# Kernel tuning notes

Hardware: AMD Instinct MI355X
Metric: run time of the kernel (lower is better)

## Reference

```python
import jax, jax.numpy as jnp
import numpy as np

N = 50000   # nodes
E = 800000  # edges
G = 64      # graphs in batch
D = 128     # joint_embed_dim
H = D // 2  # 64
NEG_SLOPE = 0.2


def _segment_softmax(logits, seg, n):
    m = jax.ops.segment_max(logits, seg, num_segments=n)
    m = jnp.where(jnp.isfinite(m), m, 0.0)
    e = jnp.exp(logits - m[seg])
    s = jax.ops.segment_sum(e, seg, num_segments=n)
    return e / (s[seg] + 1e-16)


def _gat_conv(x, src, dst, W, a_src, a_dst, b, n):
    # PyG GATConv, heads=1, add_self_loops=True
    loops = jnp.arange(n, dtype=src.dtype)
    s = jnp.concatenate([src, loops])
    d = jnp.concatenate([dst, loops])
    h = x @ W                                   # [n, out]
    alpha_s = h @ a_src                         # [n]
    alpha_d = h @ a_dst
    logit = jax.nn.leaky_relu(alpha_s[s] + alpha_d[d], NEG_SLOPE)  # [E+n]
    alpha = _segment_softmax(logit, d, n)
    out = jax.ops.segment_sum(h[s] * alpha[:, None], d, num_segments=n)
    return out + b


def _edge_conv(x, src, dst, We1, be1, We2, be2, n):
    # PyG EdgeConv: max_j nn(cat[x_i, x_j - x_i])
    xi = x[dst]
    xj = x[src]
    feats = jnp.concatenate([xi, xj - xi], axis=1)     # [E, 2*H]
    m = jax.nn.relu(feats @ We1 + be1)
    m = jax.nn.relu(m @ We2 + be2)
    out = jax.ops.segment_max(m, dst, num_segments=n)
    return jnp.where(jnp.isfinite(out), out, 0.0)


def setup_inputs() -> dict:
    key = jax.random.key(0)
    ks = jax.random.split(key, 24)
    x = jax.random.normal(ks[0], (N, 3), dtype=jnp.float32)
    edge_index = jax.random.randint(ks[1], (2, E), 0, N, dtype=jnp.int64)
    batch_ids = jnp.sort(jax.random.randint(ks[2], (N,), 0, G, dtype=jnp.int64))

    def w(k, shape, fan_in):
        return jax.random.normal(k, shape, dtype=jnp.float32) * (1.0 / np.sqrt(fan_in))

    inp = {
        "x": x, "edge_index": edge_index, "batch_ids": batch_ids,
        # GATConv1: 3 -> 64
        "W1": w(ks[3], (3, H), 3), "a1s": w(ks[4], (H,), H), "a1d": w(ks[5], (H,), H), "b1": jnp.zeros((H,), jnp.float32),
        # GATConv2: 64 -> 64
        "W2": w(ks[6], (H, H), H), "a2s": w(ks[7], (H,), H), "a2d": w(ks[8], (H,), H), "b2": jnp.zeros((H,), jnp.float32),
        # GATConv3: 128 -> 128
        "W3": w(ks[9], (D, D), D), "a3s": w(ks[10], (D,), D), "a3d": w(ks[11], (D,), D), "b3": jnp.zeros((D,), jnp.float32),
        # EdgeConv nn: 128 -> 128 -> 128
        "We1": w(ks[12], (D, D), D), "be1": jnp.zeros((D,), jnp.float32),
        "We2": w(ks[13], (D, D), D), "be2": jnp.zeros((D,), jnp.float32),
        # MLP: 256 -> 128 -> 128
        "Wm1": w(ks[14], (2 * D, D), 2 * D), "bm1": jnp.zeros((D,), jnp.float32),
        "Wm2": w(ks[15], (D, D), D), "bm2": jnp.zeros((D,), jnp.float32),
    }
    return inp


def reference(x, edge_index, batch_ids,
              W1, a1s, a1d, b1, W2, a2s, a2d, b2, W3, a3s, a3d, b3,
              We1, be1, We2, be2, Wm1, bm1, Wm2, bm2):
    src, dst = edge_index[0], edge_index[1]
    n = x.shape[0]
    # conv1 + relu (dropout is identity in eval)
    h = jax.nn.relu(_gat_conv(x, src, dst, W1, a1s, a1d, b1, n))
    # conv2 + elu
    h = jax.nn.elu(_gat_conv(h, src, dst, W2, a2s, a2d, b2, n))
    # edge_conv: 64 -> 128
    h = _edge_conv(h, src, dst, We1, be1, We2, be2, n)
    # conv3 + relu
    h = jax.nn.relu(_gat_conv(h, src, dst, W3, a3s, a3d, b3, n))
    # global mean / max pool over graphs
    sums = jax.ops.segment_sum(h, batch_ids, num_segments=G)
    cnts = jax.ops.segment_sum(jnp.ones((n, 1), h.dtype), batch_ids, num_segments=G)
    mean_pool = sums / jnp.maximum(cnts, 1.0)
    max_pool = jax.ops.segment_max(h, batch_ids, num_segments=G)
    max_pool = jnp.where(jnp.isfinite(max_pool), max_pool, 0.0)
    z = jnp.concatenate([mean_pool, max_pool], axis=1)    # [G, 256]
    z = jax.nn.relu(z @ Wm1 + bm1)
    z = jax.nn.relu(z @ Wm2 + bm2)
    norm = jnp.linalg.norm(z, axis=1, keepdims=True)
    return z / jnp.maximum(norm, 1e-12)
```

## Files before the change

kernel.cpp:

```cpp
#include <hip/hip_runtime.h>
#include <hip/hip_bf16.h>
#include <math.h>


typedef __attribute__((ext_vector_type(4))) float f32x4;
typedef __attribute__((ext_vector_type(8))) short bf16x8;
typedef __attribute__((ext_vector_type(8))) ushort u16x8;
typedef short s16x2 __attribute__((ext_vector_type(2)));

__device__ __forceinline__ float wave_sum(float v) {
#pragma unroll
  for (int o = 32; o > 0; o >>= 1) v += __shfl_xor(v, o, 64);
  return v;
}
__device__ __forceinline__ float half_sum(float v) {
#pragma unroll
  for (int o = 16; o > 0; o >>= 1) v += __shfl_xor(v, o, 64);
  return v;
}
__device__ __forceinline__ float half_max(float v) {
#pragma unroll
  for (int o = 16; o > 0; o >>= 1) v = fmaxf(v, __shfl_xor(v, o, 64));
  return v;
}
__device__ __forceinline__ float lrelu(float x) { return x >= 0.f ? x : 0.2f * x; }
__device__ __forceinline__ ushort f2bf(float f) {
  union { float f; unsigned u; } v; v.f = f;
  unsigned r = (v.u + 0x7fff + ((v.u >> 16) & 1)) >> 16;
  return (ushort)r;
}
__device__ __forceinline__ float bf2f(ushort u) {
  union { unsigned u; float f; } v; v.u = ((unsigned)u) << 16;
  return v.f;
}
__device__ __forceinline__ float bflo(unsigned v) { return __uint_as_float(v << 16); }
__device__ __forceinline__ float bfhi(unsigned v) { return __uint_as_float(v & 0xffff0000u); }
__device__ __forceinline__ unsigned pack2bf(float a, float b) {
  __hip_bfloat162 h = __float22bfloat162_rn(make_float2(a, b));
  union { __hip_bfloat162 h; unsigned u; } cv;
  cv.h = h;
  return cv.u;
}
__device__ __forceinline__ unsigned bfadd2_relu(unsigned a, unsigned b) {
  union { unsigned u; __hip_bfloat162 h; s16x2 s; } ua, ub, ur;
  ua.u = a;
  ub.u = b;
  ur.h = __hadd2(ua.h, ub.h);
  s16x2 z = (s16x2)0;
  ur.s = __builtin_elementwise_max(ur.s, z);
  return ur.u;
}


__global__ void count_kernel(const int* __restrict__ ei, int* __restrict__ deg, int E) {
  int e = blockIdx.x * 256 + threadIdx.x;
  if (e < E) atomicAdd(&deg[ei[E + e]], 1);
}

__global__ void scan_local(const int* __restrict__ deg, int* __restrict__ off,
                           int* __restrict__ bsum, int n) {
  __shared__ int buf[256];
  int i = blockIdx.x * 256 + threadIdx.x;
  int v = (i < n) ? deg[i] : 0;
  buf[threadIdx.x] = v;
  __syncthreads();
  int incl = v;
  for (int o = 1; o < 256; o <<= 1) {
    int t = (threadIdx.x >= o) ? buf[threadIdx.x - o] : 0;
    __syncthreads();
    incl += t;
    buf[threadIdx.x] = incl;
    __syncthreads();
  }
  if (i < n) off[i] = incl - v;
  if (threadIdx.x == 255) bsum[blockIdx.x] = incl;
}

__global__ void scan_bsum(int* __restrict__ bsum, int nb) {
  __shared__ int buf[256];
  int v = (threadIdx.x < nb) ? bsum[threadIdx.x] : 0;
  buf[threadIdx.x] = v;
  __syncthreads();
  int incl = v;
  for (int o = 1; o < 256; o <<= 1) {
    int t = (threadIdx.x >= o) ? buf[threadIdx.x - o] : 0;
    __syncthreads();
    incl += t;
    buf[threadIdx.x] = incl;
    __syncthreads();
  }
  if (threadIdx.x < nb) bsum[threadIdx.x] = incl - v;
}

__global__ void scan_add(int* __restrict__ off, const int* __restrict__ bsum, int n, int total) {
  int i = blockIdx.x * 256 + threadIdx.x;
  if (i < n) off[i] += bsum[blockIdx.x];
  if (i == 0) off[n] = total;
}

__global__ void scatter_kernel(const int* __restrict__ ei, const int* __restrict__ off,
                               int* __restrict__ cursor, int* __restrict__ csr_src,
                               int* __restrict__ csr_dst, int E) {
  int e = blockIdx.x * 256 + threadIdx.x;
  if (e < E) {
    int d = ei[E + e];
    int pos = off[d] + atomicAdd(&cursor[d], 1);
    csr_src[pos] = ei[e];
    csr_dst[pos] = d;
  }
}


template <int IN, int OUT>
__global__ __launch_bounds__(256) void node_linear_kernel(
    const float* __restrict__ x, const float* __restrict__ W,
    const float* __restrict__ av_s, const float* __restrict__ av_d,
    ushort* __restrict__ hb, float* __restrict__ as_out, float* __restrict__ ad_out, int n) {
  constexpr int NC = OUT / 64;
  constexpr int NB = 4;
  __shared__ float Wl[IN * OUT];
  if constexpr ((IN * OUT) % 1024 == 0) {
    for (int i = threadIdx.x; i < IN * OUT / 4; i += 256)
      ((float4*)Wl)[i] = ((const float4*)W)[i];
  } else {
    for (int i = threadIdx.x; i < IN * OUT; i += 256) Wl[i] = W[i];
  }
  __syncthreads();
  const int wid = threadIdx.x >> 6, lane = threadIdx.x & 63;
  const int n0 = (blockIdx.x * 4 + wid) * NB;
  if (n0 >= n) return;
  float acc[NB][NC];
#pragma unroll
  for (int j = 0; j < NB; ++j)
#pragma unroll
    for (int c = 0; c < NC; ++c) acc[j][c] = 0.f;
  int nidx[NB];
#pragma unroll
  for (int j = 0; j < NB; ++j) nidx[j] = min(n0 + j, n - 1);

  if constexpr ((IN & 3) == 0) {
#pragma unroll 2
    for (int k = 0; k < IN; k += 4) {
      float4 xv[NB];
#pragma unroll
      for (int j = 0; j < NB; ++j) xv[j] = *(const float4*)&x[nidx[j] * IN + k];
#pragma unroll
      for (int kk = 0; kk < 4; ++kk) {
        float w[NC];
        if constexpr (NC == 2) {
          float2 wv = *(const float2*)&Wl[(k + kk) * OUT + 2 * lane];
          w[0] = wv.x;
          w[1] = wv.y;
        } else {
          w[0] = Wl[(k + kk) * OUT + lane];
        }
#pragma unroll
        for (int j = 0; j < NB; ++j) {
          float xk = (kk == 0) ? xv[j].x : (kk == 1) ? xv[j].y : (kk == 2) ? xv[j].z : xv[j].w;
#pragma unroll
          for (int c = 0; c < NC; ++c) acc[j][c] += xk * w[c];
        }
      }
    }
  } else {
    for (int k = 0; k < IN; ++k) {
      float w[NC];
#pragma unroll
      for (int c = 0; c < NC; ++c) w[c] = (NC == 2) ? Wl[k * OUT + 2 * lane + c] : Wl[k * OUT + lane];
#pragma unroll
      for (int j = 0; j < NB; ++j) {
        float xk = x[nidx[j] * IN + k];
#pragma unroll
        for (int c = 0; c < NC; ++c) acc[j][c] += xk * w[c];
      }
    }
  }

  float a_sv[NC], a_dv[NC];
#pragma unroll
  for (int c = 0; c < NC; ++c) {
    const int col = (NC == 2) ? 2 * lane + c : lane;
    a_sv[c] = av_s[col];
    a_dv[c] = av_d[col];
  }
#pragma unroll
  for (int j = 0; j < NB; ++j) {
    int node = n0 + j;
    if (node >= n) break;
    float ps = 0.f, pd = 0.f;
#pragma unroll
    for (int c = 0; c < NC; ++c) {
      ps += acc[j][c] * a_sv[c];
      pd += acc[j][c] * a_dv[c];
    }
    if constexpr (NC == 2) {
      unsigned pk = pack2bf(acc[j][0], acc[j][1]);
      *(unsigned*)&hb[(size_t)node * OUT + 2 * lane] = pk;
    } else {
      hb[(size_t)node * OUT + lane] = f2bf(acc[j][0]);
    }
    ps = wave_sum(ps);
    pd = wave_sum(pd);
    if (lane == 0) {
      as_out[node] = ps;
      ad_out[node] = pd;
    }
  }
}


template <int K>
__global__ void compute_wa(const float* __restrict__ W, const float* __restrict__ a_s,
                           const float* __restrict__ a_d, float* __restrict__ wa_s,
                           float* __restrict__ wa_d) {
  const int k = threadIdx.x;
  float s = 0.f, d = 0.f;
  for (int j = 0; j < K; ++j) {
    const float w = W[k * K + j];
    s += w * a_s[j];
    d += w * a_d[j];
  }
  wa_s[k] = s;
  wa_d[k] = d;
}


#define NT 64
#define M1S 136
#define M2S 132

__global__ __launch_bounds__(256, 4) void node_mfma_kernel(
    const float* __restrict__ x, const ushort* __restrict__ Wcm,
    const float* __restrict__ wa_s, const float* __restrict__ wa_d,
    ushort* __restrict__ hb, float* __restrict__ as_out, float* __restrict__ ad_out, int n) {
  __shared__ __align__(16) char smem[NT * M2S * 4];
  __shared__ float swa[128], swd[128];
  ushort* m1 = (ushort*)smem;
  float* m2 = (float*)smem;
  const int tid = threadIdx.x;
  const int lane = tid & 63, wid = tid >> 6;
  const int quad = lane >> 4, l16 = lane & 15;
  const int row = tid >> 2, c0 = (tid & 3) * 32;

  bf16x8 bfrag[2][4];
#pragma unroll
  for (int ct = 0; ct < 2; ++ct) {
    const int nn = wid * 32 + ct * 16 + l16;
#pragma unroll
    for (int ks = 0; ks < 4; ++ks)
      bfrag[ct][ks] = *(const bf16x8*)&Wcm[nn * 128 + ks * 32 + quad * 8];
  }
  if (tid < 128) {
    swa[tid] = wa_s[tid];
    swd[tid] = wa_d[tid];
  }
  __syncthreads();

  const int n0 = blockIdx.x * NT;
  const int node = min(n0 + row, n - 1);

  float ps = 0.f, pd = 0.f;
  {
    const float4* xp = (const float4*)&x[(size_t)node * 128 + c0];
#pragma unroll
    for (int i = 0; i < 4; ++i) {
      const float4 a = xp[2 * i], b = xp[2 * i + 1];
      const float4 wa0 = *(const float4*)&swa[c0 + 8 * i];
      const float4 wa1 = *(const float4*)&swa[c0 + 8 * i + 4];
      const float4 wd0 = *(const float4*)&swd[c0 + 8 * i];
      const float4 wd1 = *(const float4*)&swd[c0 + 8 * i + 4];
      ps += a.x * wa0.x + a.y * wa0.y + a.z * wa0.z + a.w * wa0.w
          + b.x * wa1.x + b.y * wa1.y + b.z * wa1.z + b.w * wa1.w;
      pd += a.x * wd0.x + a.y * wd0.y + a.z * wd0.z + a.w * wd0.w
          + b.x * wd1.x + b.y * wd1.y + b.z * wd1.z + b.w * wd1.w;
      uint4 rr;
      rr.x = pack2bf(a.x, a.y);
      rr.y = pack2bf(a.z, a.w);
      rr.z = pack2bf(b.x, b.y);
      rr.w = pack2bf(b.z, b.w);
      *((uint4*)&m1[row * M1S + c0] + i) = rr;
    }
  }
  ps += __shfl_xor(ps, 1, 64);
  ps += __shfl_xor(ps, 2, 64);
  pd += __shfl_xor(pd, 1, 64);
  pd += __shfl_xor(pd, 2, 64);
  if ((tid & 3) == 0 && n0 + row < n) {
    as_out[n0 + row] = ps;
    ad_out[n0 + row] = pd;
  }
  __syncthreads();

  f32x4 acc[4][2];
#pragma unroll
  for (int rt = 0; rt < 4; ++rt)
#pragma unroll
    for (int ct = 0; ct < 2; ++ct) acc[rt][ct] = (f32x4)0.f;
#pragma unroll
  for (int ks = 0; ks < 4; ++ks) {
    bf16x8 afr[4];
#pragma unroll
    for (int rt = 0; rt < 4; ++rt)
      afr[rt] = *(const bf16x8*)&m1[(rt * 16 + l16) * M1S + ks * 32 + quad * 8];
#pragma unroll
    for (int rt = 0; rt < 4; ++rt)
#pragma unroll
// ... 47 lines not shown
#pragma unroll
  for (int ks = 0; ks < 2; ++ks)
    bfrag[ks] = *(const bf16x8*)&Wcm[(wid * 16 + l16) * 64 + ks * 32 + quad * 8];
  if (tid < 64) {
    swa[tid] = wa_s[tid];
    swd[tid] = wa_d[tid];
  }
  __syncthreads();

  const int n0 = blockIdx.x * NT;
  const int node = min(n0 + row, n - 1);

  float ps = 0.f, pd = 0.f;
  {
    const float4* xp = (const float4*)&x[(size_t)node * 64 + c0];
#pragma unroll
    for (int i = 0; i < 2; ++i) {
      const float4 a = xp[2 * i], b = xp[2 * i + 1];
      const float4 wa0 = *(const float4*)&swa[c0 + 8 * i];
      const float4 wa1 = *(const float4*)&swa[c0 + 8 * i + 4];
      const float4 wd0 = *(const float4*)&swd[c0 + 8 * i];
      const float4 wd1 = *(const float4*)&swd[c0 + 8 * i + 4];
      ps += a.x * wa0.x + a.y * wa0.y + a.z * wa0.z + a.w * wa0.w
          + b.x * wa1.x + b.y * wa1.y + b.z * wa1.z + b.w * wa1.w;
      pd += a.x * wd0.x + a.y * wd0.y + a.z * wd0.z + a.w * wd0.w
          + b.x * wd1.x + b.y * wd1.y + b.z * wd1.z + b.w * wd1.w;
      uint4 rr;
      rr.x = pack2bf(a.x, a.y);
      rr.y = pack2bf(a.z, a.w);
      rr.z = pack2bf(b.x, b.y);
      rr.w = pack2bf(b.z, b.w);
      *((uint4*)&m1[row * M1S64 + c0] + i) = rr;
    }
  }
  ps += __shfl_xor(ps, 1, 64);
  ps += __shfl_xor(ps, 2, 64);
  pd += __shfl_xor(pd, 1, 64);
  pd += __shfl_xor(pd, 2, 64);
  if ((tid & 3) == 0 && n0 + row < n) {
    as_out[n0 + row] = ps;
    ad_out[n0 + row] = pd;
  }
  __syncthreads();

  f32x4 acc[4];
#pragma unroll
  for (int rt = 0; rt < 4; ++rt) acc[rt] = (f32x4)0.f;
#pragma unroll
  for (int ks = 0; ks < 2; ++ks) {
    bf16x8 afr[4];
#pragma unroll
    for (int rt = 0; rt < 4; ++rt)
      afr[rt] = *(const bf16x8*)&m1[(rt * 16 + l16) * M1S64 + ks * 32 + quad * 8];
#pragma unroll
    for (int rt = 0; rt < 4; ++rt)
      acc[rt] = __builtin_amdgcn_mfma_f32_16x16x32_bf16(afr[rt], bfrag[ks], acc[rt], 0, 0, 0);
  }
  __syncthreads();

  {
    const int col = wid * 16 + l16;
#pragma unroll
    for (int rt = 0; rt < 4; ++rt)
#pragma unroll
      for (int r = 0; r < 4; ++r) {
        const int rr2 = rt * 16 + quad * 4 + r;
        m2[rr2 * M2S64 + col] = acc[rt][r];
      }
  }
  __syncthreads();

  unsigned* hbu = (unsigned*)hb;
#pragma unroll
  for (int i = 0; i < 8; ++i) {
    const int r = wid * 2 + (lane >> 5) + 8 * i;
    const int j = lane & 31;
    if (n0 + r < n)
      hbu[(size_t)(n0 + r) * 32 + j] =
          pack2bf(m2[r * M2S64 + 2 * j], m2[r * M2S64 + 2 * j + 1]);
  }
}


template <int ACT>
__global__ __launch_bounds__(256) void gat_agg128h_kernel(
    const ushort* __restrict__ h, const float* __restrict__ as_, const float* __restrict__ ad_,
    const float* __restrict__ bias, const int* __restrict__ off, const int* __restrict__ csr_src,
    float* __restrict__ out, int n) {
  __shared__ float wbuf[4][64];
  __shared__ int sbuf[4][64];
  const int wid = threadIdx.x >> 6, lane = threadIdx.x & 63;
  const int half = lane >> 5, sl = lane & 31;
  const int d0 = blockIdx.x * 8 + wid * 2 + half;
  const bool wr = d0 < n;
  const int d = wr ? d0 : (n - 1);
  const int s0 = off[d], s1 = off[d + 1];
  const float ad = ad_[d];
  const float l_self = lrelu(as_[d] + ad);
  const uint2 selfv = *(const uint2*)&h[(size_t)d * 128 + 4 * sl];

  float m = l_self;
  float esum_l = 0.f, acc0 = 0.f, acc1 = 0.f, acc2 = 0.f, acc3 = 0.f;

  for (int base = s0; base < s1; base += 32) {
    const int cnt = min(32, s1 - base);
    const int idx = base + sl;
    float l = -3.0e38f;
    int s_l = 0;
    if (idx < s1) {
      s_l = csr_src[idx];
      l = lrelu(as_[s_l] + ad);
    }
    const float cm = half_max(l);
    const float alpha = (cm > m) ? __expf(m - cm) : 1.f;
    esum_l *= alpha;
    acc0 *= alpha;
    acc1 *= alpha;
    acc2 *= alpha;
    acc3 *= alpha;
    m = fmaxf(m, cm);
    const float w_l = (idx < s1) ? __expf(l - m) : 0.f;
    sbuf[wid][half * 32 + sl] = s_l;
    wbuf[wid][half * 32 + sl] = w_l;
    esum_l += w_l;
    __threadfence_block();
    int j = 0;
    for (; j + 8 <= cnt; j += 8) {
      float w[8];
      int a[8];
#pragma unroll
      for (int t = 0; t < 8; ++t) {
        w[t] = wbuf[wid][half * 32 + j + t];
        a[t] = sbuf[wid][half * 32 + j + t];
      }
      uint2 v[8];
#pragma unroll
      for (int t = 0; t < 8; ++t) v[t] = *(const uint2*)&h[(size_t)a[t] * 128 + 4 * sl];
#pragma unroll
      for (int t = 0; t < 8; ++t) {
        acc0 += w[t] * bflo(v[t].x);
        acc1 += w[t] * bfhi(v[t].x);
        acc2 += w[t] * bflo(v[t].y);
        acc3 += w[t] * bfhi(v[t].y);
      }
    }
    for (; j < cnt; ++j) {
      const float wj = wbuf[wid][half * 32 + j];
      const int aj = sbuf[wid][half * 32 + j];
      const uint2 v = *(const uint2*)&h[(size_t)aj * 128 + 4 * sl];
      acc0 += wj * bflo(v.x);
      acc1 += wj * bfhi(v.x);
      acc2 += wj * bflo(v.y);
      acc3 += wj * bfhi(v.y);
    }
    __threadfence_block();
  }
  const float self_w = __expf(l_self - m);
  const float esum = half_sum(esum_l) + self_w;
  acc0 += self_w * bflo(selfv.x);
  acc1 += self_w * bfhi(selfv.x);
  acc2 += self_w * bflo(selfv.y);
  acc3 += self_w * bfhi(selfv.y);
  const float inv = 1.f / (esum + 1e-16f);
  float v0 = acc0 * inv + bias[4 * sl];
  float v1 = acc1 * inv + bias[4 * sl + 1];
  float v2 = acc2 * inv + bias[4 * sl + 2];
  float v3 = acc3 * inv + bias[4 * sl + 3];
  if (ACT == 0) {
    v0 = fmaxf(v0, 0.f);
    v1 = fmaxf(v1, 0.f);
    v2 = fmaxf(v2, 0.f);
    v3 = fmaxf(v3, 0.f);
  } else {
    v0 = v0 > 0.f ? v0 : expm1f(v0);
    v1 = v1 > 0.f ? v1 : expm1f(v1);
    v2 = v2 > 0.f ? v2 : expm1f(v2);
    v3 = v3 > 0.f ? v3 : expm1f(v3);
  }
  if (wr) {
    float4 o4;
    o4.x = v0;
    o4.y = v1;
    o4.z = v2;
    o4.w = v3;
    *(float4*)&out[(size_t)d * 128 + 4 * sl] = o4;
  }
}


template <int ACT>
__global__ __launch_bounds__(256) void gat_agg64_kernel(
    const ushort* __restrict__ h, const float* __restrict__ as_, const float* __restrict__ ad_,
    const float* __restrict__ bias, const int* __restrict__ off, const int* __restrict__ csr_src,
    float* __restrict__ out, int n) {
  __shared__ float wbuf[4][64];
  __shared__ int sbuf[4][64];
  const int wid = threadIdx.x >> 6, lane = threadIdx.x & 63;
  const int half = lane >> 5, sl = lane & 31;
  const int d0 = blockIdx.x * 8 + wid * 2 + half;
  const bool wr = d0 < n;
  const int d = wr ? d0 : (n - 1);
  const int s0 = off[d], s1 = off[d + 1];
  const float ad = ad_[d];
  const float l_self = lrelu(as_[d] + ad);
  const unsigned selfv = *(const unsigned*)&h[(size_t)d * 64 + 2 * sl];

  float m = l_self;
  float esum_l = 0.f, acc0 = 0.f, acc1 = 0.f;

  for (int base = s0; base < s1; base += 32) {
    const int cnt = min(32, s1 - base);
    const int idx = base + sl;
    float l = -3.0e38f;
    int s_l = 0;
    if (idx < s1) {
      s_l = csr_src[idx];
      l = lrelu(as_[s_l] + ad);
    }
    const float cm = half_max(l);
    const float alpha = (cm > m) ? __expf(m - cm) : 1.f;
    esum_l *= alpha;
    acc0 *= alpha;
    acc1 *= alpha;
    m = fmaxf(m, cm);
    const float w_l = (idx < s1) ? __expf(l - m) : 0.f;
    sbuf[wid][half * 32 + sl] = s_l;
    wbuf[wid][half * 32 + sl] = w_l;
    esum_l += w_l;
    __threadfence_block();
    int j = 0;
    for (; j + 8 <= cnt; j += 8) {
      float w[8];
      int a[8];
#pragma unroll
      for (int t = 0; t < 8; ++t) {
        w[t] = wbuf[wid][half * 32 + j + t];
        a[t] = sbuf[wid][half * 32 + j + t];
      }
      unsigned v[8];
#pragma unroll
      for (int t = 0; t < 8; ++t) v[t] = *(const unsigned*)&h[(size_t)a[t] * 64 + 2 * sl];
#pragma unroll
      for (int t = 0; t < 8; ++t) {
        acc0 += w[t] * bflo(v[t]);
        acc1 += w[t] * bfhi(v[t]);
      }
    }
    for (; j < cnt; ++j) {
      const float wj = wbuf[wid][half * 32 + j];
      const int aj = sbuf[wid][half * 32 + j];
      const unsigned v = *(const unsigned*)&h[(size_t)aj * 64 + 2 * sl];
      acc0 += wj * bflo(v);
      acc1 += wj * bfhi(v);
    }
    __threadfence_block();
  }
  const float self_w = __expf(l_self - m);
  const float esum = half_sum(esum_l) + self_w;
  acc0 += self_w * bflo(selfv);
  acc1 += self_w * bfhi(selfv);
  const float inv = 1.f / (esum + 1e-16f);
  float v0 = acc0 * inv + bias[2 * sl];
  float v1 = acc1 * inv + bias[2 * sl + 1];
  if (ACT == 0) {
    v0 = fmaxf(v0, 0.f);
    v1 = fmaxf(v1, 0.f);
  } else {
    v0 = v0 > 0.f ? v0 : expm1f(v0);
    v1 = v1 > 0.f ? v1 : expm1f(v1);
  }
  if (wr) *(float2*)&out[(size_t)d * 64 + 2 * sl] = make_float2(v0, v1);
}


__global__ __launch_bounds__(256) void pq_kernel(
    const float* __restrict__ x, const float* __restrict__ We1, const float* __restrict__ be1,
    ushort* __restrict__ P, ushort* __restrict__ Q, int n) {
  __shared__ float AmB[64 * 128];
  __shared__ float Bm[64 * 128];
  for (int i = threadIdx.x; i < 64 * 128; i += 256) {
    float b = We1[64 * 128 + i];
    AmB[i] = We1[i] - b;
    Bm[i] = b;
  }
  __syncthreads();
  const int wid = threadIdx.x >> 6, lane = threadIdx.x & 63;
  const int n0 = (blockIdx.x * 4 + wid) * 4;
  if (n0 >= n) return;
  int nidx[4];
#pragma unroll
  for (int j = 0; j < 4; ++j) nidx[j] = min(n0 + j, n - 1);
  float ap[4][2], aq[4][2];
#pragma unroll
  for (int j = 0; j < 4; ++j) { ap[j][0] = ap[j][1] = aq[j][0] = aq[j][1] = 0.f; }
#pragma unroll 2
  for (int k = 0; k < 64; k += 4) {
    float4 xv[4];
#pragma unroll
    for (int j = 0; j < 4; ++j) xv[j] = *(const float4*)&x[nidx[j] * 64 + k];
#pragma unroll
    for (int kk = 0; kk < 4; ++kk) {
      const float wa0 = AmB[(k + kk) * 128 + lane], wa1 = AmB[(k + kk) * 128 + 64 + lane];
      const float wb0 = Bm[(k + kk) * 128 + lane], wb1 = Bm[(k + kk) * 128 + 64 + lane];
#pragma unroll
      for (int j = 0; j < 4; ++j) {
        const float xk = (kk == 0) ? xv[j].x : (kk == 1) ? xv[j].y : (kk == 2) ? xv[j].z : xv[j].w;
        ap[j][0] += xk * wa0;
        ap[j][1] += xk * wa1;
        aq[j][0] += xk * wb0;
        aq[j][1] += xk * wb1;
      }
    }
  }
  const float b0 = be1[lane], b1v = be1[64 + lane];
#pragma unroll
  for (int j = 0; j < 4; ++j) {
    const int node = n0 + j;
    if (node >= n) break;
    P[(size_t)node * 128 + lane] = f2bf(ap[j][0] + b0);
    P[(size_t)node * 128 + 64 + lane] = f2bf(ap[j][1] + b1v);
    Q[(size_t)node * 128 + lane] = f2bf(aq[j][0]);
    Q[(size_t)node * 128 + 64 + lane] = f2bf(aq[j][1]);
  }
}


template <int K>
__global__ void convert_wcm(const float* __restrict__ W, ushort* __restrict__ Wcm) {
  int i = blockIdx.x * 256 + threadIdx.x;
  if (i >= K * K) return;
  int k = i / K, nn = i % K;
  Wcm[nn * K + k] = f2bf(W[k * K + nn]);
}


#define TE 64
#define M2T 68

__global__ __launch_bounds__(256, 4) void edgeconv_mfma_kernel(
    const int* __restrict__ csr_src, const int* __restrict__ csr_dst,
    const ushort* __restrict__ P, const ushort* __restrict__ Q,
    const ushort* __restrict__ We2cm, const float* __restrict__ be2,
    float* __restrict__ out, int E, int ntiles) {
  __shared__ __align__(16) char smem[128 * M2T * 4];
  __shared__ __align__(16) int didx2[2][TE];
  ushort* m1 = (ushort*)smem;
  float* m2t = (float*)smem;
  const int tid = threadIdx.x;
  const int lane = tid & 63, wid = tid >> 6;
  const int quad = lane >> 4, l16 = lane & 15;
  const int row = tid >> 2;
  const int c0 = (tid & 3) * 32;

  bf16x8 bfrag[2][4];
#pragma unroll
  for (int ct = 0; ct < 2; ++ct) {
    const int nn = wid * 32 + ct * 16 + l16;
#pragma unroll
    for (int ks = 0; ks < 4; ++ks)
      bfrag[ct][ks] = *(const bf16x8*)&We2cm[nn * 128 + ks * 32 + quad * 8];
  }
  const float b0v = be2[wid * 32 + l16];
  const float b1v = be2[wid * 32 + 16 + l16];

  int t = blockIdx.x;
  if (t >= ntiles) return;

  uint4 pv[4], qv[4];
  {
    const int p = t * TE + row;
    int dd = 0, ss = 0;
    if (p < E) { dd = csr_dst[p]; ss = csr_src[p]; }
    const uint4* Pp = (const uint4*)&P[(size_t)dd * 128 + c0];
    const uint4* Qp = (const uint4*)&Q[(size_t)ss * 128 + c0];
#pragma unroll
    for (int i = 0; i < 4; ++i) { pv[i] = Pp[i]; qv[i] = Qp[i]; }
  }
  if (tid < TE) {
    const int p = t * TE + tid;
    didx2[0][tid] = (p < E) ? csr_dst[p] : -1;
  }

  int buf = 0;
  for (; t < ntiles; t += gridDim.x, buf ^= 1) {
    __syncthreads();

#pragma unroll
    for (int i = 0; i < 4; ++i) {
      uint4 rr;
      rr.x = bfadd2_relu(pv[i].x, qv[i].x);
      rr.y = bfadd2_relu(pv[i].y, qv[i].y);
      rr.z = bfadd2_relu(pv[i].z, qv[i].z);
      rr.w = bfadd2_relu(pv[i].w, qv[i].w);
      *((uint4*)&m1[row * M1S + c0] + i) = rr;
    }

    const int tn = t + gridDim.x;
    const bool hasNext = (tn < ntiles);
    int ddn = 0, ssn = 0;
    if (hasNext) {
      const int p = tn * TE + row;
      if (p < E) { ddn = csr_dst[p]; ssn = csr_src[p]; }
      if (tid < TE) {
        const int p2 = tn * TE + tid;
        didx2[buf ^ 1][tid] = (p2 < E) ? csr_dst[p2] : -1;
      }
    }
    __syncthreads();

    f32x4 acc[4][2];
#pragma unroll
    for (int rt = 0; rt < 4; ++rt)
#pragma unroll
      for (int ct = 0; ct < 2; ++ct) acc[rt][ct] = (f32x4)0.f;
#pragma unroll
// ... 97 lines not shown
    const int* __restrict__ bid, int n,
    const float* __restrict__ Wm1, const float* __restrict__ bm1,
    const float* __restrict__ Wm2, const float* __restrict__ bm2,
    float* __restrict__ outp) {
  const int g = blockIdx.x;
  const int c = threadIdx.x;
  __shared__ float zin[256], z1[128];
  __shared__ int scnt;
  if (c == 0) {
    int lo = 0, hi = n;
    while (lo < hi) { int mid = (lo + hi) >> 1; if (bid[mid] < g) lo = mid + 1; else hi = mid; }
    const int start = lo;
    lo = start; hi = n;
    while (lo < hi) { int mid = (lo + hi) >> 1; if (bid[mid] < g + 1) lo = mid + 1; else hi = mid; }
    scnt = lo - start;
  }
  __syncthreads();
  const float invc = 1.f / fmaxf((float)scnt, 1.f);
  zin[c] = psum[g * 128 + c] * invc;
  zin[c + 128] = pmax[g * 128 + c];
  __syncthreads();
  float a = bm1[c];
  for (int k = 0; k < 256; ++k) a += zin[k] * Wm1[k * 128 + c];
  a = fmaxf(a, 0.f);
  z1[c] = a;
  __syncthreads();
  float b = bm2[c];
  for (int k = 0; k < 128; ++k) b += z1[k] * Wm2[k * 128 + c];
  b = fmaxf(b, 0.f);
  float ss = wave_sum(b * b);
  __shared__ float sred[2];
  if ((threadIdx.x & 63) == 0) sred[threadIdx.x >> 6] = ss;
  __syncthreads();
  const float nrm = sqrtf(sred[0] + sred[1]);
  outp[g * 128 + c] = b / fmaxf(nrm, 1e-12f);
}


extern "C" void kernel_launch(void* const* d_in, const int* in_sizes, int n_in, void* d_out,
                              int out_size, void* d_ws, size_t ws_size, hipStream_t stream) {
  const float* x = (const float*)d_in[0];
  const int* ei = (const int*)d_in[1];
  const int* bid = (const int*)d_in[2];
  const float* W1 = (const float*)d_in[3];
  const float* a1s = (const float*)d_in[4];
  const float* a1d = (const float*)d_in[5];
  const float* b1 = (const float*)d_in[6];
  const float* W2 = (const float*)d_in[7];
  const float* a2s = (const float*)d_in[8];
  const float* a2d = (const float*)d_in[9];
  const float* b2 = (const float*)d_in[10];
  const float* W3 = (const float*)d_in[11];
  const float* a3s = (const float*)d_in[12];
  const float* a3d = (const float*)d_in[13];
  const float* b3 = (const float*)d_in[14];
  const float* We1 = (const float*)d_in[15];
  const float* be1 = (const float*)d_in[16];
  const float* We2 = (const float*)d_in[17];
  const float* be2 = (const float*)d_in[18];
  const float* Wm1 = (const float*)d_in[19];
  const float* bm1 = (const float*)d_in[20];
  const float* Wm2 = (const float*)d_in[21];
  const float* bm2v = (const float*)d_in[22];

  const int n = in_sizes[0] / 3;
  const int E = in_sizes[1] / 2;
  const int G = out_size / 128;

  char* w = (char*)d_ws;
  size_t o = 0;
  auto alloc = [&](size_t bytes) {
    void* p = w + o;
    o = (o + bytes + 255) & ~(size_t)255;
    return p;
  };
  int* deg = (int*)alloc((size_t)n * 4);
  int* off = (int*)alloc((size_t)(n + 1) * 4);
  int* bsum = (int*)alloc(1024 * 4);
  int* csr_src = (int*)alloc((size_t)E * 4);
  int* csr_dst = (int*)alloc((size_t)E * 4);
  ushort* We2cm = (ushort*)alloc(128 * 128 * 2);
  ushort* W3cm = (ushort*)alloc(128 * 128 * 2);
  ushort* W2cm = (ushort*)alloc(64 * 64 * 2);
  float* was = (float*)alloc(128 * 4);
  float* wad = (float*)alloc(128 * 4);
  float* wa2s = (float*)alloc(64 * 4);
  float* wa2d = (float*)alloc(64 * 4);
  float* as_ = (float*)alloc((size_t)n * 4);
  float* ad_ = (float*)alloc((size_t)n * 4);
  ushort* T64 = (ushort*)alloc((size_t)n * 64 * 2);
  float* X64 = (float*)alloc((size_t)n * 64 * 4);
  ushort* Pbf = (ushort*)alloc((size_t)n * 128 * 2);
  ushort* Qbf = (ushort*)alloc((size_t)n * 128 * 2);
  float* H3 = (float*)alloc((size_t)n * 128 * 4);
  float* psum = (float*)alloc((size_t)G * 128 * 4);
  float* pmax = (float*)alloc((size_t)G * 128 * 4);
  (void)ws_size;

  ushort* Hbf = Pbf;
  float* C3out = H3;

  const int nb256 = (n + 255) / 256;
  const int ebl = (E + 255) / 256;
  const int nlb = (n + 15) / 16;
  const int agb8 = (n + 7) / 8;
  const int ecb = (E + TE - 1) / TE;
  const int nmb = (n + NT - 1) / NT;

  hipMemsetAsync(deg, 0, (size_t)n * 4, stream);
  count_kernel<<<ebl, 256, 0, stream>>>(ei, deg, E);
  scan_local<<<nb256, 256, 0, stream>>>(deg, off, bsum, n);
  scan_bsum<<<1, 256, 0, stream>>>(bsum, nb256);
  scan_add<<<nb256, 256, 0, stream>>>(off, bsum, n, E);
  hipMemsetAsync(deg, 0, (size_t)n * 4, stream);
  scatter_kernel<<<ebl, 256, 0, stream>>>(ei, off, deg, csr_src, csr_dst, E);
  convert_wcm<128><<<64, 256, 0, stream>>>(We2, We2cm);
  convert_wcm<128><<<64, 256, 0, stream>>>(W3, W3cm);
  convert_wcm<64><<<16, 256, 0, stream>>>(W2, W2cm);
  compute_wa<128><<<1, 128, 0, stream>>>(W3, a3s, a3d, was, wad);
  compute_wa<64><<<1, 64, 0, stream>>>(W2, a2s, a2d, wa2s, wa2d);

  node_linear_kernel<3, 64><<<nlb, 256, 0, stream>>>(x, W1, a1s, a1d, T64, as_, ad_, n);
  gat_agg64_kernel<0><<<agb8, 256, 0, stream>>>(T64, as_, ad_, b1, off, csr_src, X64, n);
  node_mfma64_kernel<<<nmb, 256, 0, stream>>>(X64, W2cm, wa2s, wa2d, T64, as_, ad_, n);
  gat_agg64_kernel<1><<<agb8, 256, 0, stream>>>(T64, as_, ad_, b2, off, csr_src, X64, n);
  pq_kernel<<<nlb, 256, 0, stream>>>(X64, We1, be1, Pbf, Qbf, n);
  hipMemsetAsync(H3, 0, (size_t)n * 128 * 4, stream);
  edgeconv_mfma_kernel<<<1024, 256, 0, stream>>>(csr_src, csr_dst, Pbf, Qbf, We2cm, be2, H3,
                                                 E, ecb);
  node_mfma_kernel<<<nmb, 256, 0, stream>>>(H3, W3cm, was, wad, Hbf, as_, ad_, n);
  gat_agg128h_kernel<0><<<agb8, 256, 0, stream>>>(Hbf, as_, ad_, b3, off, csr_src, C3out, n);
  hipMemsetAsync(psum, 0, (size_t)G * 128 * 4 * 2, stream);
  pool_part_kernel<<<512, 256, 0, stream>>>(C3out, bid, psum, pmax, n);
  mlp_kernel<<<G, 128, 0, stream>>>(psum, pmax, bid, n, Wm1, bm1, Wm2, bm2v, (float*)d_out);
}
```

Measured before the change: 485.4 us.

## Fuse prep kernels, MFMA the PQ projection, and drop online-max softmax rescaling

The weight conversions, attention-vector folds and the memsets of deg, H3 and the pool buffers are merged into one prep kernel, which removes several small launches. The CSR scatter now decrements the degree counters with atomicSub instead of resetting a cursor array, so the second memset is gone. The scalar pq_kernel is replaced by a bf16 MFMA kernel that multiplies against a precombined weight matrix. The GAT aggregation no longer keeps a running max; it normalises each edge logit by the self-loop logit. That saves the max reduction and the rescale work per chunk, but it can overflow if a neighbour's logit is far above the self logit.

Result: faster. 444.7 us (-8.4%).

```diff
diff --git a/kernel.cpp b/kernel.cpp
--- a/kernel.cpp
+++ b/kernel.cpp
@@ -5,7 +5,6 @@
 
 typedef __attribute__((ext_vector_type(4))) float f32x4;
 typedef __attribute__((ext_vector_type(8))) short bf16x8;
-typedef __attribute__((ext_vector_type(8))) ushort u16x8;
 typedef short s16x2 __attribute__((ext_vector_type(2)));
 
 __device__ __forceinline__ float wave_sum(float v) {
@@ -16,11 +15,6 @@
 __device__ __forceinline__ float half_sum(float v) {
 #pragma unroll
   for (int o = 16; o > 0; o >>= 1) v += __shfl_xor(v, o, 64);
-  return v;
-}
-__device__ __forceinline__ float half_max(float v) {
-#pragma unroll
-  for (int o = 16; o > 0; o >>= 1) v = fmaxf(v, __shfl_xor(v, o, 64));
   return v;
 }
 __device__ __forceinline__ float lrelu(float x) { return x >= 0.f ? x : 0.2f * x; }
@@ -28,10 +22,6 @@
   union { float f; unsigned u; } v; v.f = f;
   unsigned r = (v.u + 0x7fff + ((v.u >> 16) & 1)) >> 16;
   return (ushort)r;
-}
-__device__ __forceinline__ float bf2f(ushort u) {
-  union { unsigned u; float f; } v; v.u = ((unsigned)u) << 16;
-  return v.f;
 }
 __device__ __forceinline__ float bflo(unsigned v) { return __uint_as_float(v << 16); }
 __device__ __forceinline__ float bfhi(unsigned v) { return __uint_as_float(v & 0xffff0000u); }
@@ -52,6 +42,66 @@
 }
 
 
+__global__ void prep_kernel(const float* __restrict__ We1, const float* __restrict__ We2,
+                            const float* __restrict__ W2, const float* __restrict__ W3,
+                            const float* __restrict__ a2s, const float* __restrict__ a2d,
+                            const float* __restrict__ a3s, const float* __restrict__ a3d,
+                            ushort* __restrict__ Wpqcm, ushort* __restrict__ We2cm,
+                            ushort* __restrict__ W2cm, ushort* __restrict__ W3cm,
+                            float* __restrict__ wa2s, float* __restrict__ wa2d,
+                            float* __restrict__ wa3s, float* __restrict__ wa3d,
+                            int* __restrict__ deg, float* __restrict__ H3,
+                            float* __restrict__ psum2, int n, int G) {
+  const int b = blockIdx.x, tid = threadIdx.x;
+  if (b < 64) {
+    const int i = b * 256 + tid, j = i >> 6, k = i & 63;
+    const float v = (j < 128) ? (We1[k * 128 + j] - We1[(64 + k) * 128 + j])
+                              : We1[(64 + k) * 128 + (j - 128)];
+    Wpqcm[j * 64 + k] = f2bf(v);
+  } else if (b < 128) {
+    const int i = (b - 64) * 256 + tid, k = i >> 7, c = i & 127;
+    We2cm[c * 128 + k] = f2bf(We2[k * 128 + c]);
+  } else if (b < 192) {
+    const int i = (b - 128) * 256 + tid, k = i >> 7, c = i & 127;
+    W3cm[c * 128 + k] = f2bf(W3[k * 128 + c]);
+  } else if (b < 208) {
+    const int i = (b - 192) * 256 + tid, k = i >> 6, c = i & 63;
+    W2cm[c * 64 + k] = f2bf(W2[k * 64 + c]);
+  } else if (b == 208) {
+    if (tid < 128) {
+      float s = 0.f, d = 0.f;
+      for (int j = 0; j < 128; ++j) {
+        const float w = W3[tid * 128 + j];
+        s += w * a3s[j];
+        d += w * a3d[j];
+      }
+      wa3s[tid] = s;
+      wa3d[tid] = d;
+    }
+  } else if (b == 209) {
+    if (tid < 64) {
+      float s = 0.f, d = 0.f;
+      for (int j = 0; j < 64; ++j) {
+        const float w = W2[tid * 64 + j];
+        s += w * a2s[j];
+        d += w * a2d[j];
+      }
+      wa2s[tid] = s;
+      wa2d[tid] = d;
+    }
+  } else {
+    const int gtid = (b - 210) * 256 + tid;
+    const int stride = (gridDim.x - 210) * 256;
+    for (int i = gtid; i < n; i += stride) deg[i] = 0;
+    const uint4 z = {0, 0, 0, 0};
+    uint4* H4 = (uint4*)H3;
+    for (int i = gtid; i < n * 32; i += stride) H4[i] = z;
+    uint4* P4 = (uint4*)psum2;
+    for (int i = gtid; i < G * 64; i += stride) P4[i] = z;
+  }
+}
+
+
 __global__ void count_kernel(const int* __restrict__ ei, int* __restrict__ deg, int E) {
   int e = blockIdx.x * 256 + threadIdx.x;
   if (e < E) atomicAdd(&deg[ei[E + e]], 1);
@@ -99,12 +149,12 @@
 }
 
 __global__ void scatter_kernel(const int* __restrict__ ei, const int* __restrict__ off,
-                               int* __restrict__ cursor, int* __restrict__ csr_src,
+                               int* __restrict__ deg, int* __restrict__ csr_src,
                                int* __restrict__ csr_dst, int E) {
   int e = blockIdx.x * 256 + threadIdx.x;
   if (e < E) {
     int d = ei[E + e];
-    int pos = off[d] + atomicAdd(&cursor[d], 1);
+    int pos = off[d] + atomicSub(&deg[d], 1) - 1;
     csr_src[pos] = ei[e];
     csr_dst[pos] = d;
   }
@@ -116,89 +166,33 @@
     const float* __restrict__ x, const float* __restrict__ W,
     const float* __restrict__ av_s, const float* __restrict__ av_d,
     ushort* __restrict__ hb, float* __restrict__ as_out, float* __restrict__ ad_out, int n) {
-  constexpr int NC = OUT / 64;
   constexpr int NB = 4;
   __shared__ float Wl[IN * OUT];
-  if constexpr ((IN * OUT) % 1024 == 0) {
-    for (int i = threadIdx.x; i < IN * OUT / 4; i += 256)
-      ((float4*)Wl)[i] = ((const float4*)W)[i];
-  } else {
-    for (int i = threadIdx.x; i < IN * OUT; i += 256) Wl[i] = W[i];
-  }
+  for (int i = threadIdx.x; i < IN * OUT; i += 256) Wl[i] = W[i];
   __syncthreads();
   const int wid = threadIdx.x >> 6, lane = threadIdx.x & 63;
   const int n0 = (blockIdx.x * 4 + wid) * NB;
   if (n0 >= n) return;
-  float acc[NB][NC];
-#pragma unroll
-  for (int j = 0; j < NB; ++j)
-#pragma unroll
-    for (int c = 0; c < NC; ++c) acc[j][c] = 0.f;
+  float acc[NB];
+#pragma unroll
+  for (int j = 0; j < NB; ++j) acc[j] = 0.f;
   int nidx[NB];
 #pragma unroll
   for (int j = 0; j < NB; ++j) nidx[j] = min(n0 + j, n - 1);
 
-  if constexpr ((IN & 3) == 0) {
-#pragma unroll 2
-    for (int k = 0; k < IN; k += 4) {
-      float4 xv[NB];
-#pragma unroll
-      for (int j = 0; j < NB; ++j) xv[j] = *(const float4*)&x[nidx[j] * IN + k];
-#pragma unroll
-      for (int kk = 0; kk < 4; ++kk) {
-        float w[NC];
-        if constexpr (NC == 2) {
-          float2 wv = *(const float2*)&Wl[(k + kk) * OUT + 2 * lane];
-          w[0] = wv.x;
-          w[1] = wv.y;
-        } else {
-          w[0] = Wl[(k + kk) * OUT + lane];
-        }
-#pragma unroll
-        for (int j = 0; j < NB; ++j) {
-          float xk = (kk == 0) ? xv[j].x : (kk == 1) ? xv[j].y : (kk == 2) ? xv[j].z : xv[j].w;
-#pragma unroll
-          for (int c = 0; c < NC; ++c) acc[j][c] += xk * w[c];
-        }
-      }
-    }
-  } else {
-    for (int k = 0; k < IN; ++k) {
-      float w[NC];
-#pragma unroll
-      for (int c = 0; c < NC; ++c) w[c] = (NC == 2) ? Wl[k * OUT + 2 * lane + c] : Wl[k * OUT + lane];
-#pragma unroll
-      for (int j = 0; j < NB; ++j) {
-        float xk = x[nidx[j] * IN + k];
-#pragma unroll
-        for (int c = 0; c < NC; ++c) acc[j][c] += xk * w[c];
-      }
-    }
-  }
-
-  float a_sv[NC], a_dv[NC];
-#pragma unroll
-  for (int c = 0; c < NC; ++c) {
-    const int col = (NC == 2) ? 2 * lane + c : lane;
-    a_sv[c] = av_s[col];
-    a_dv[c] = av_d[col];
-  }
+  for (int k = 0; k < IN; ++k) {
+    const float w = Wl[k * OUT + lane];
+#pragma unroll
+    for (int j = 0; j < NB; ++j) acc[j] += x[nidx[j] * IN + k] * w;
+  }
+
+  const float a_sv = av_s[lane], a_dv = av_d[lane];
 #pragma unroll
   for (int j = 0; j < NB; ++j) {
     int node = n0 + j;
     if (node >= n) break;
-    float ps = 0.f, pd = 0.f;
-#pragma unroll
-    for (int c = 0; c < NC; ++c) {
-      ps += acc[j][c] * a_sv[c];
-      pd += acc[j][c] * a_dv[c];
-    }
-    if constexpr (NC == 2) {
-      unsigned pk = pack2bf(acc[j][0], acc[j][1]);
-      *(unsigned*)&hb[(size_t)node * OUT + 2 * lane] = pk;
-    } else {
-      hb[(size_t)node * OUT + lane] = f2bf(acc[j][0]);
-    }
+    float ps = acc[j] * a_sv, pd = acc[j] * a_dv;
+    hb[(size_t)node * OUT + lane] = f2bf(acc[j]);
     ps = wave_sum(ps);
     pd = wave_sum(pd);
     if (lane == 0) {
@@ -206,22 +200,6 @@
       ad_out[node] = pd;
     }
   }
-}
-
-
-template <int K>
-__global__ void compute_wa(const float* __restrict__ W, const float* __restrict__ a_s,
-                           const float* __restrict__ a_d, float* __restrict__ wa_s,
-                           float* __restrict__ wa_d) {
-  const int k = threadIdx.x;
-  float s = 0.f, d = 0.f;
-  for (int j = 0; j < K; ++j) {
-    const float w = W[k * K + j];
-    s += w * a_s[j];
-    d += w * a_d[j];
-  }
-  wa_s[k] = s;
-  wa_d[k] = d;
 }
 
 
@@ -435,6 +413,116 @@
 }
 
 
+#define MPQ 132
+
+__global__ __launch_bounds__(256) void pq_mfma_kernel(
+    const float* __restrict__ x, const ushort* __restrict__ Wpqcm,
+    const float* __restrict__ be1, ushort* __restrict__ P, ushort* __restrict__ Q, int n) {
+  __shared__ __align__(16) char smem[NT * MPQ * 4];
+  __shared__ float sbias[128];
+  ushort* m1 = (ushort*)smem;
+  float* m2 = (float*)smem;
+  const int tid = threadIdx.x;
+  const int lane = tid & 63, wid = tid >> 6;
+  const int quad = lane >> 4, l16 = lane & 15;
+  const int row = tid >> 2, c0 = (tid & 3) * 16;
+
+  bf16x8 bfrag[4][2];
+#pragma unroll
+  for (int ct = 0; ct < 4; ++ct)
+#pragma unroll
+    for (int ks = 0; ks < 2; ++ks)
+      bfrag[ct][ks] =
+          *(const bf16x8*)&Wpqcm[(wid * 64 + ct * 16 + l16) * 64 + ks * 32 + quad * 8];
+  if (tid < 128) sbias[tid] = be1[tid];
+
+  const int n0 = blockIdx.x * NT;
+  const int node = min(n0 + row, n - 1);
+  {
+    const float4* xp = (const float4*)&x[(size_t)node * 64 + c0];
+#pragma unroll
+    for (int i = 0; i < 2; ++i) {
+      const float4 a = xp[2 * i], b = xp[2 * i + 1];
+      uint4 rr;
+      rr.x = pack2bf(a.x, a.y);
+      rr.y = pack2bf(a.z, a.w);
+      rr.z = pack2bf(b.x, b.y);
+      rr.w = pack2bf(b.z, b.w);
+      *((uint4*)&m1[row * M1S64 + c0] + i) = rr;
+    }
+  }
+  __syncthreads();
+
+  f32x4 acc[4][4];
+#pragma unroll
+  for (int rt = 0; rt < 4; ++rt)
+#pragma unroll
+    for (int ct = 0; ct < 4; ++ct) acc[rt][ct] = (f32x4)0.f;
+#pragma unroll
+  for (int ks = 0; ks < 2; ++ks) {
+    bf16x8 afr[4];
+#pragma unroll
+    for (int rt = 0; rt < 4; ++rt)
+      afr[rt] = *(const bf16x8*)&m1[(rt * 16 + l16) * M1S64 + ks * 32 + quad * 8];
+#pragma unroll
+    for (int rt = 0; rt < 4; ++rt)
+#pragma unroll
+      for (int ct = 0; ct < 4; ++ct)
+        acc[rt][ct] = __builtin_amdgcn_mfma_f32_16x16x32_bf16(afr[rt], bfrag[ct][ks],
+                                                              acc[rt][ct], 0, 0, 0);
+  }
+  __syncthreads();
+
+  if (wid < 2) {
+#pragma unroll
+    for (int ct = 0; ct < 4; ++ct) {
+      const int col = wid * 64 + ct * 16 + l16;
+#pragma unroll
+      for (int rt = 0; rt < 4; ++rt)
+#pragma unroll
+        for (int r = 0; r < 4; ++r)
+          m2[(rt * 16 + quad * 4 + r) * MPQ + col] = acc[rt][ct][r];
+    }
+  }
+  __syncthreads();
+  {
+    unsigned* Pu = (unsigned*)P;
+#pragma unroll
+    for (int i = 0; i < 16; ++i) {
+      const int idx = i * 256 + tid;
+      const int rw = idx >> 6, j = idx & 63;
+      if (n0 + rw < n)
+        Pu[(size_t)(n0 + rw) * 64 + j] = pack2bf(m2[rw * MPQ + 2 * j] + sbias[2 * j],
+                                                 m2[rw * MPQ + 2 * j + 1] + sbias[2 * j + 1]);
+    }
+  }
+  __syncthreads();
+  if (wid >= 2) {
+#pragma unroll
+    for (int ct = 0; ct < 4; ++ct) {
+      const int col = (wid - 2) * 64 + ct * 16 + l16;
+#pragma unroll
+      for (int rt = 0; rt < 4; ++rt)
+#pragma unroll
+        for (int r = 0; r < 4; ++r)
+          m2[(rt * 16 + quad * 4 + r) * MPQ + col] = acc[rt][ct][r];
+    }
+  }
+  __syncthreads();
+  {
+    unsigned* Qu = (unsigned*)Q;
+#pragma unroll
+    for (int i = 0; i < 16; ++i) {
+      const int idx = i * 256 + tid;
+      const int rw = idx >> 6, j = idx & 63;
+      if (n0 + rw < n)
+        Qu[(size_t)(n0 + rw) * 64 + j] =
+            pack2bf(m2[rw * MPQ + 2 * j], m2[rw * MPQ + 2 * j + 1]);
+    }
+  }
+}
+
+
 template <int ACT>
 __global__ __launch_bounds__(256) void gat_agg128h_kernel(
     const ushort* __restrict__ h, const float* __restrict__ as_, const float* __restrict__ ad_,
@@ -452,27 +540,17 @@
   const float l_self = lrelu(as_[d] + ad);
   const uint2 selfv = *(const uint2*)&h[(size_t)d * 128 + 4 * sl];
 
-  float m = l_self;
   float esum_l = 0.f, acc0 = 0.f, acc1 = 0.f, acc2 = 0.f, acc3 = 0.f;
 
   for (int base = s0; base < s1; base += 32) {
     const int cnt = min(32, s1 - base);
     const int idx = base + sl;
-    float l = -3.0e38f;
+    float w_l = 0.f;
     int s_l = 0;
     if (idx < s1) {
       s_l = csr_src[idx];
-      l = lrelu(as_[s_l] + ad);
-    }
-    const float cm = half_max(l);
-    const float alpha = (cm > m) ? __expf(m - cm) : 1.f;
-    esum_l *= alpha;
-    acc0 *= alpha;
-    acc1 *= alpha;
-    acc2 *= alpha;
-    acc3 *= alpha;
-    m = fmaxf(m, cm);
-    const float w_l = (idx < s1) ? __expf(l - m) : 0.f;
+      w_l = __expf(lrelu(as_[s_l] + ad) - l_self);
+    }
     sbuf[wid][half * 32 + sl] = s_l;
     wbuf[wid][half * 32 + sl] = w_l;
     esum_l += w_l;
@@ -508,12 +586,11 @@
     }
     __threadfence_block();
   }
-  const float self_w = __expf(l_self - m);
-  const float esum = half_sum(esum_l) + self_w;
-  acc0 += self_w * bflo(selfv.x);
-  acc1 += self_w * bfhi(selfv.x);
-  acc2 += self_w * bflo(selfv.y);
-  acc3 += self_w * bfhi(selfv.y);
+  const float esum = half_sum(esum_l) + 1.f;
+  acc0 += bflo(selfv.x);
+  acc1 += bfhi(selfv.x);
+  acc2 += bflo(selfv.y);
+  acc3 += bfhi(selfv.y);
   const float inv = 1.f / (esum + 1e-16f);
   float v0 = acc0 * inv + bias[4 * sl];
   float v1 = acc1 * inv + bias[4 * sl + 1];
@@ -558,25 +635,17 @@
   const float l_self = lrelu(as_[d] + ad);
   const unsigned selfv = *(const unsigned*)&h[(size_t)d * 64 + 2 * sl];
 
-  float m = l_self;
   float esum_l = 0.f, acc0 = 0.f, acc1 = 0.f;
 
   for (int base = s0; base < s1; base += 32) {
     const int cnt = min(32, s1 - base);
     const int idx = base + sl;
-    float l = -3.0e38f;
+    float w_l = 0.f;
     int s_l = 0;
     if (idx < s1) {
       s_l = csr_src[idx];
-      l = lrelu(as_[s_l] + ad);
-    }
-    const float cm = half_max(l);
-    const float alpha = (cm > m) ? __expf(m - cm) : 1.f;
-    esum_l *= alpha;
-    acc0 *= alpha;
-    acc1 *= alpha;
-    m = fmaxf(m, cm);
-    const float w_l = (idx < s1) ? __expf(l - m) : 0.f;
+      w_l = __expf(lrelu(as_[s_l] + ad) - l_self);
+    }
     sbuf[wid][half * 32 + sl] = s_l;
     wbuf[wid][half * 32 + sl] = w_l;
     esum_l += w_l;
@@ -608,10 +677,9 @@
     }
     __threadfence_block();
   }
-  const float self_w = __expf(l_self - m);
-  const float esum = half_sum(esum_l) + self_w;
-  acc0 += self_w * bflo(selfv);
-  acc1 += self_w * bfhi(selfv);
+  const float esum = half_sum(esum_l) + 1.f;
+  acc0 += bflo(selfv);
+  acc1 += bfhi(selfv);
   const float inv = 1.f / (esum + 1e-16f);
   float v0 = acc0 * inv + bias[2 * sl];
   float v1 = acc1 * inv + bias[2 * sl + 1];
@@ -623,67 +691,6 @@
     v1 = v1 > 0.f ? v1 : expm1f(v1);
   }
   if (wr) *(float2*)&out[(size_t)d * 64 + 2 * sl] = make_float2(v0, v1);
-}
-
-
-__global__ __launch_bounds__(256) void pq_kernel(
-    const float* __restrict__ x, const float* __restrict__ We1, const float* __restrict__ be1,
-    ushort* __restrict__ P, ushort* __restrict__ Q, int n) {
-  __shared__ float AmB[64 * 128];
-  __shared__ float Bm[64 * 128];
-  for (int i = threadIdx.x; i < 64 * 128; i += 256) {
-    float b = We1[64 * 128 + i];
-    AmB[i] = We1[i] - b;
-    Bm[i] = b;
-  }
-  __syncthreads();
-  const int wid = threadIdx.x >> 6, lane = threadIdx.x & 63;
-  const int n0 = (blockIdx.x * 4 + wid) * 4;
-  if (n0 >= n) return;
-  int nidx[4];
-#pragma unroll
-  for (int j = 0; j < 4; ++j) nidx[j] = min(n0 + j, n - 1);
-  float ap[4][2], aq[4][2];
-#pragma unroll
-  for (int j = 0; j < 4; ++j) { ap[j][0] = ap[j][1] = aq[j][0] = aq[j][1] = 0.f; }
-#pragma unroll 2
-  for (int k = 0; k < 64; k += 4) {
-    float4 xv[4];
-#pragma unroll
-    for (int j = 0; j < 4; ++j) xv[j] = *(const float4*)&x[nidx[j] * 64 + k];
-#pragma unroll
-    for (int kk = 0; kk < 4; ++kk) {
-      const float wa0 = AmB[(k + kk) * 128 + lane], wa1 = AmB[(k + kk) * 128 + 64 + lane];
-      const float wb0 = Bm[(k + kk) * 128 + lane], wb1 = Bm[(k + kk) * 128 + 64 + lane];
-#pragma unroll
-      for (int j = 0; j < 4; ++j) {
-        const float xk = (kk == 0) ? xv[j].x : (kk == 1) ? xv[j].y : (kk == 2) ? xv[j].z : xv[j].w;
-        ap[j][0] += xk * wa0;
-        ap[j][1] += xk * wa1;
-        aq[j][0] += xk * wb0;
-        aq[j][1] += xk * wb1;
-      }
-    }
-  }
-  const float b0 = be1[lane], b1v = be1[64 + lane];
-#pragma unroll
-  for (int j = 0; j < 4; ++j) {
-    const int node = n0 + j;
-    if (node >= n) break;
-    P[(size_t)node * 128 + lane] = f2bf(ap[j][0] + b0);
-    P[(size_t)node * 128 + 64 + lane] = f2bf(ap[j][1] + b1v);
-    Q[(size_t)node * 128 + lane] = f2bf(aq[j][0]);
-    Q[(size_t)node * 128 + 64 + lane] = f2bf(aq[j][1]);
-  }
-}
-
-
-template <int K>
-__global__ void convert_wcm(const float* __restrict__ W, ushort* __restrict__ Wcm) {
-  int i = blockIdx.x * 256 + threadIdx.x;
-  if (i >= K * K) return;
-  int k = i / K, nn = i % K;
-  Wcm[nn * K + k] = f2bf(W[k * K + nn]);
 }
 
 
@@ -947,8 +954,9 @@
   ushort* We2cm = (ushort*)alloc(128 * 128 * 2);
   ushort* W3cm = (ushort*)alloc(128 * 128 * 2);
   ushort* W2cm = (ushort*)alloc(64 * 64 * 2);
-  float* was = (float*)alloc(128 * 4);
-  float* wad = (float*)alloc(128 * 4);
+  ushort* Wpqcm = (ushort*)alloc(256 * 64 * 2);
+  float* wa3s = (float*)alloc(128 * 4);
+  float* wa3d = (float*)alloc(128 * 4);
   float* wa2s = (float*)alloc(64 * 4);
   float* wa2d = (float*)alloc(64 * 4);
   float* as_ = (float*)alloc((size_t)n * 4);
@@ -972,30 +980,23 @@
   const int ecb = (E + TE - 1) / TE;
   const int nmb = (n + NT - 1) / NT;
 
-  hipMemsetAsync(deg, 0, (size_t)n * 4, stream);
+  prep_kernel<<<1024, 256, 0, stream>>>(We1, We2, W2, W3, a2s, a2d, a3s, a3d, Wpqcm, We2cm,
+                                        W2cm, W3cm, wa2s, wa2d, wa3s, wa3d, deg, H3, psum, n, G);
   count_kernel<<<ebl, 256, 0, stream>>>(ei, deg, E);
   scan_local<<<nb256, 256, 0, stream>>>(deg, off, bsum, n);
   scan_bsum<<<1, 256, 0, stream>>>(bsum, nb256);
   scan_add<<<nb256, 256, 0, stream>>>(off, bsum, n, E);
-  hipMemsetAsync(deg, 0, (size_t)n * 4, stream);
   scatter_kernel<<<ebl, 256, 0, stream>>>(ei, off, deg, csr_src, csr_dst, E);
-  convert_wcm<128><<<64, 256, 0, stream>>>(We2, We2cm);
-  convert_wcm<128><<<64, 256, 0, stream>>>(W3, W3cm);
-  convert_wcm<64><<<16, 256, 0, stream>>>(W2, W2cm);
-  compute_wa<128><<<1, 128, 0, stream>>>(W3, a3s, a3d, was, wad);
-  compute_wa<64><<<1, 64, 0, stream>>>(W2, a2s, a2d, wa2s, wa2d);
 
   node_linear_kernel<3, 64><<<nlb, 256, 0, stream>>>(x, W1, a1s, a1d, T64, as_, ad_, n);
   gat_agg64_kernel<0><<<agb8, 256, 0, stream>>>(T64, as_, ad_, b1, off, csr_src, X64, n);
   node_mfma64_kernel<<<nmb, 256, 0, stream>>>(X64, W2cm, wa2s, wa2d, T64, as_, ad_, n);
   gat_agg64_kernel<1><<<agb8, 256, 0, stream>>>(T64, as_, ad_, b2, off, csr_src, X64, n);
-  pq_kernel<<<nlb, 256, 0, stream>>>(X64, We1, be1, Pbf, Qbf, n);
-  hipMemsetAsync(H3, 0, (size_t)n * 128 * 4, stream);
+  pq_mfma_kernel<<<nmb, 256, 0, stream>>>(X64, Wpqcm, be1, Pbf, Qbf, n);
   edgeconv_mfma_kernel<<<1024, 256, 0, stream>>>(csr_src, csr_dst, Pbf, Qbf, We2cm, be2, H3,
                                                  E, ecb);
-  node_mfma_kernel<<<nmb, 256, 0, stream>>>(H3, W3cm, was, wad, Hbf, as_, ad_, n);
+  node_mfma_kernel<<<nmb, 256, 0, stream>>>(H3, W3cm, wa3s, wa3d, Hbf, as_, ad_, n);
   gat_agg128h_kernel<0><<<agb8, 256, 0, stream>>>(Hbf, as_, ad_, b3, off, csr_src, C3out, n);
-  hipMemsetAsync(psum, 0, (size_t)G * 128 * 4 * 2, stream);
   pool_part_kernel<<<512, 256, 0, stream>>>(C3out, bid, psum, pmax, n);
   mlp_kernel<<<G, 128, 0, stream>>>(psum, pmax, bid, n, Wm1, bm1, Wm2, bm2v, (float*)d_out);
 }
```
